# Optimization experiments

Hardware: AMD Instinct MI355X
Metric: run time of the kernel (lower is better)

Reference implementation:

```python
import jax, jax.numpy as jnp
import numpy as np
from jax import lax

B, NC, NF = 16, 1024, 4096   # clouds, coarse pts/cloud, fine pts/cloud
C_IN, C_SKIP, C_HID, K = 256, 128, 256, 3
BN_EPS = 1e-5


def setup_inputs() -> dict:
    key = jax.random.key(0)
    ks = jax.random.split(key, 12)
    inp = {
        "x": jax.random.normal(ks[0], (B * NC, C_IN), jnp.float32),
        "pos": jax.random.normal(ks[1], (B * NC, 3), jnp.float32),
        "batch": jnp.arange(B * NC, dtype=jnp.int64) // NC,
        "x_skip": jax.random.normal(ks[2], (B * NF, C_SKIP), jnp.float32),
        "pos_skip": jax.random.normal(ks[3], (B * NF, 3), jnp.float32),
        "batch_skip": jnp.arange(B * NF, dtype=jnp.int64) // NF,
    }
    d_in = C_IN + C_SKIP
    inp["W1"] = jax.random.normal(ks[4], (d_in, C_HID), jnp.float32) / np.sqrt(d_in)
    inp["b1"] = jnp.zeros((C_HID,), jnp.float32)
    inp["g1"] = jnp.ones((C_HID,), jnp.float32)
    inp["be1"] = jnp.zeros((C_HID,), jnp.float32)
    inp["W2"] = jax.random.normal(ks[5], (C_HID, C_HID), jnp.float32) / np.sqrt(C_HID)
    inp["b2"] = jnp.zeros((C_HID,), jnp.float32)
    inp["g2"] = jnp.ones((C_HID,), jnp.float32)
    inp["be2"] = jnp.zeros((C_HID,), jnp.float32)
    return inp


def _knn_interpolate(x, pos, pos_skip):
    # batches are contiguous equal-size -> reshape per cloud
    xb = x.reshape(B, NC, C_IN)
    pc = pos.reshape(B, NC, 3)
    pf = pos_skip.reshape(B, NF, 3)
    # squared distances [B, NF, NC]
    d2 = jnp.sum((pf[:, :, None, :] - pc[:, None, :, :]) ** 2, axis=-1)
    neg_d, idx = lax.top_k(-d2, K)                      # [B, NF, K]
    w = 1.0 / jnp.maximum(-neg_d, 1e-16)                # inverse-squared-distance weights
    feats = xb[jnp.arange(B)[:, None, None], idx]       # [B, NF, K, C_IN]
    out = jnp.sum(w[..., None] * feats, axis=2) / jnp.sum(w, axis=2, keepdims=True)
    return out.reshape(B * NF, C_IN)


def _mlp_layer(h, W, b, g, be):
    z = jax.nn.relu(h @ W + b)
    mean = jnp.mean(z, axis=0)
    var = jnp.mean((z - mean) ** 2, axis=0)            # biased var, as torch BN
    return (z - mean) * lax.rsqrt(var + BN_EPS) * g + be


def reference(x, pos, batch, x_skip, pos_skip, batch_skip,
              W1, b1, g1, be1, W2, b2, g2, be2):
    h = _knn_interpolate(x, pos, pos_skip)
    h = jnp.concatenate([h, x_skip], axis=1)            # [B*NF, C_IN+C_SKIP]
    h = _mlp_layer(h, W1, b1, g1, be1)
    h = _mlp_layer(h, W2, b2, g2, be2)
    return h
```

## Files before the change

kernel.cpp:

```cpp
#include <hip/hip_runtime.h>
#include <hip/hip_bf16.h>

#define NB    16
#define NC    1024
#define NF    4096
#define MROWS 65536
#define CIN   256
#define CSK   128
#define DIN   384
#define CHID  256
#define BN_EPS 1e-5f

typedef __attribute__((ext_vector_type(8))) short bf16x8;
typedef __attribute__((ext_vector_type(4))) float f32x4;
typedef __attribute__((ext_vector_type(2))) float f32x2;

__device__ __forceinline__ unsigned short f2bfu(float f) {
  __hip_bfloat16 h = __float2bfloat16(f);
  return __builtin_bit_cast(unsigned short, h);
}
__device__ __forceinline__ float bfu2f(unsigned short u) {
  unsigned int w = ((unsigned int)u) << 16;
  return __builtin_bit_cast(float, w);
}

__device__ __forceinline__ void load_lds16(const void* g, void* lds) {
  __builtin_amdgcn_global_load_lds(
      (const __attribute__((address_space(1))) unsigned int*)g,
      (__attribute__((address_space(3))) unsigned int*)lds, 16, 0, 0);
}

__device__ __forceinline__ void ins3(float d2, int j, float& b0, float& b1,
                                     float& b2v, int& i0, int& i1, int& i2) {
  const bool c0 = d2 < b0, c1 = d2 < b1, c2 = d2 < b2v;
  const float nb1 = __builtin_amdgcn_fmed3f(d2, b0, b1);
  const float nb2 = __builtin_amdgcn_fmed3f(d2, b1, b2v);
  i2  = c1 ? i1 : (c2 ? j : i2);
  i1  = c0 ? i0 : (c1 ? j : i1);
  i0  = c0 ? j : i0;
  b2v = nb2;
  b1  = nb1;
  b0  = fminf(d2, b0);
}

__global__ __launch_bounds__(512) void knn_interp_kernel(
    const float* __restrict__ x,
    const float* __restrict__ pos,
    const float* __restrict__ x_skip,
    const float* __restrict__ pos_skip,
    __hip_bfloat16* __restrict__ h0,
    const float* __restrict__ W1,
    __hip_bfloat16* __restrict__ W1t,
    float* __restrict__ stats)
{
  const int tid = threadIdx.x, wid = tid >> 6, lane = tid & 63;

  if (blockIdx.x >= 1024) {
    const int c = blockIdx.x - 1024;
    if (c == 0 && tid < 256) {
      for (int k = tid; k < 1024; k += 256) stats[k] = 0.f;
    }
    if (tid < 256)
      W1t[(size_t)tid * DIN + c] = __float2bfloat16(W1[(size_t)c * CHID + tid]);
    return;
  }

  __shared__ f32x4 nxy[512];
  __shared__ f32x2 nz[512];
  __shared__ float  md[8][64][3];
  __shared__ int    mi[8][64][3];
  __shared__ float  fw[64][3];
  __shared__ int    fi[64][3];

  const int f0 = blockIdx.x * 64;
  const int b  = f0 >> 12;

  const float* pb = pos + (size_t)b * NC * 3;
  for (int j = tid; j < 512; j += 512) {
    const float* p = pb + 6 * j;
    nxy[j] = (f32x4){-p[0], -p[3], -p[1], -p[4]};
    nz[j]  = (f32x2){-p[2], -p[5]};
  }
  __syncthreads();

  const int f = f0 + lane;
  const float* pf = pos_skip + (size_t)f * 3;
  const float fx = pf[0], fy = pf[1], fz = pf[2];
  const f32x4 fxxyy = (f32x4){fx, fx, fy, fy};
  const f32x2 fzz = (f32x2){fz, fz};

  float b0 = 3.4e38f, b1 = 3.4e38f, b2v = 3.4e38f;
  int   i0 = 0, i1 = 0, i2 = 0;
  const int pbase = wid * 64;
#pragma unroll 4
  for (int p = 0; p < 64; ++p) {
    const f32x4 cxy = nxy[pbase + p];
    const f32x2 cz  = nz[pbase + p];
    f32x2 d2;
    {
#pragma clang fp contract(off)
      const f32x4 dxy = fxxyy + cxy;
      const f32x4 sq  = dxy * dxy;
      const f32x2 sxy = (f32x2){sq[0], sq[1]} + (f32x2){sq[2], sq[3]};
      const f32x2 dz  = fzz + cz;
      d2 = sxy + dz * dz;
    }
    const int j = 2 * (pbase + p);
    ins3(d2[0], j,     b0, b1, b2v, i0, i1, i2);
    ins3(d2[1], j + 1, b0, b1, b2v, i0, i1, i2);
  }
  md[wid][lane][0] = b0;  md[wid][lane][1] = b1;  md[wid][lane][2] = b2v;
  mi[wid][lane][0] = i0;  mi[wid][lane][1] = i1;  mi[wid][lane][2] = i2;
  __syncthreads();

  if (wid == 0) {
#pragma unroll
    for (int q = 1; q < 8; ++q)
#pragma unroll
      for (int e = 0; e < 3; ++e)
        ins3(md[q][lane][e], mi[q][lane][e], b0, b1, b2v, i0, i1, i2);

    float w0 = 1.f / fmaxf(b0, 1e-16f);
    float w1 = 1.f / fmaxf(b1, 1e-16f);
    float w2 = 1.f / fmaxf(b2v, 1e-16f);
    const float inv = 1.f / (w0 + w1 + w2);
    fw[lane][0] = w0 * inv; fw[lane][1] = w1 * inv; fw[lane][2] = w2 * inv;
    fi[lane][0] = i0; fi[lane][1] = i1; fi[lane][2] = i2;
  }
  __syncthreads();

  for (int pp = 0; pp < 8; ++pp) {
    const int p = wid * 8 + pp;
    const float w0 = fw[p][0], w1 = fw[p][1], w2 = fw[p][2];
    const int j0 = fi[p][0], j1 = fi[p][1], j2 = fi[p][2];
    const float4* r0 = (const float4*)(x + (size_t)(b * NC + j0) * CIN);
    const float4* r1 = (const float4*)(x + (size_t)(b * NC + j1) * CIN);
    const float4* r2 = (const float4*)(x + (size_t)(b * NC + j2) * CIN);
    const float4 a0 = r0[lane], a1 = r1[lane], a2 = r2[lane];
    float4 v;
    v.x = w0 * a0.x + w1 * a1.x + w2 * a2.x;
    v.y = w0 * a0.y + w1 * a1.y + w2 * a2.y;
    v.z = w0 * a0.z + w1 * a1.z + w2 * a2.z;
    v.w = w0 * a0.w + w1 * a1.w + w2 * a2.w;
    __hip_bfloat16* orow = h0 + (size_t)(f0 + p) * DIN;
    ushort4 o;
    o.x = f2bfu(v.x); o.y = f2bfu(v.y); o.z = f2bfu(v.z); o.w = f2bfu(v.w);
    ((ushort4*)orow)[lane] = o;
    const float2 s = ((const float2*)(x_skip + (size_t)(f0 + p) * CSK))[lane];
    const unsigned int packed =
        ((unsigned int)f2bfu(s.y) << 16) | (unsigned int)f2bfu(s.x);
    ((unsigned int*)(orow + CIN))[lane] = packed;
  }
}

__global__ __launch_bounds__(256) void prep_w2b2_kernel(
    const float* __restrict__ W2, const float* __restrict__ stats,
    const float* __restrict__ g1, const float* __restrict__ be1,
    const float* __restrict__ b2, __hip_bfloat16* __restrict__ W2t,
    float* __restrict__ b2p) {
  const int n = blockIdx.x, c = threadIdx.x;
  const int wid = c >> 6, lane = c & 63;
  const float m = stats[c] * (1.f / MROWS);
  const float var = stats[256 + c] * (1.f / MROWS) - m * m;
  const float sc = g1[c] * rsqrtf(var + BN_EPS);
  const float sh = be1[c] - m * sc;
  const float w = W2[(size_t)c * CHID + n];
  W2t[(size_t)n * CHID + c] = __float2bfloat16(sc * w);
  float p = sh * w;
#pragma unroll
  for (int off = 32; off > 0; off >>= 1) p += __shfl_down(p, off);
  __shared__ float red4[4];
  if (lane == 0) red4[wid] = p;
  __syncthreads();
  if (c == 0) b2p[n] = red4[0] + red4[1] + red4[2] + red4[3] + b2[n];
}

template<int KD>
__global__ __launch_bounds__(512) void gemm_bias_relu(
    const __hip_bfloat16* __restrict__ A,
    const __hip_bfloat16* __restrict__ Bt,
    const float* __restrict__ bias,
    __hip_bfloat16* __restrict__ out,
    float* __restrict__ gsum,
    float* __restrict__ gsq)
{
  __shared__ __hip_bfloat16 As[2 * 128 * 32];
  __shared__ __hip_bfloat16 Bs[2 * 256 * 32];
  __shared__ float ssum[256], ssq[256];
  const int tid = threadIdx.x;
  const int wid = tid >> 6, lane = tid & 63;
  const int bm = blockIdx.x;
  const int wr = wid >> 2, wc = wid & 3;
  const int la = lane & 15, lk = lane >> 4;

  if (tid < 256) { ssum[tid] = 0.f; ssq[tid] = 0.f; }

  f32x4 acc[4][4] = {};

  const int rA = tid >> 2;
  const int c8 = (tid & 3) * 8;
  const __hip_bfloat16* gA  = A  + (size_t)(bm * 128 + rA) * KD + c8;
  const __hip_bfloat16* gB0 = Bt + (size_t)rA * KD + c8;
  const __hip_bfloat16* gB1 = Bt + (size_t)(128 + rA) * KD + c8;
  char* ldsA  = (char*)As + wid * 1024;
  char* ldsB0 = (char*)Bs + wid * 1024;

  load_lds16(gA,       ldsA);
  load_lds16(gB0,      ldsB0);
  load_lds16(gB1,      ldsB0 + 8192);
  __syncthreads();

  const int nIter = KD / 32;
  for (int it = 0; it < nIter; ++it) {
    const int cur = it & 1, nxt = cur ^ 1;
    if (it + 1 < nIter) {
      const int k1 = (it + 1) * 32;
      load_lds16(gA  + k1, ldsA  + nxt * 8192);
      load_lds16(gB0 + k1, ldsB0 + nxt * 16384);
      load_lds16(gB1 + k1, ldsB0 + nxt * 16384 + 8192);
    }
    const __hip_bfloat16* Acur = As + cur * 4096;
    const __hip_bfloat16* Bcur = Bs + cur * 8192;
    bf16x8 af[4], bfr[4];
#pragma unroll
    for (int m = 0; m < 4; ++m)
      af[m] = *(const bf16x8*)(Acur + (wr * 64 + m * 16 + la) * 32 + lk * 8);
#pragma unroll
    for (int n = 0; n < 4; ++n)
      bfr[n] = *(const bf16x8*)(Bcur + (wc * 64 + n * 16 + la) * 32 + lk * 8);
#pragma unroll
    for (int m = 0; m < 4; ++m)
#pragma unroll
      for (int n = 0; n < 4; ++n)
        acc[m][n] = __builtin_amdgcn_mfma_f32_16x16x32_bf16(
            af[m], bfr[n], acc[m][n], 0, 0, 0);
    __syncthreads();
  }

  const int rowBase = bm * 128 + wr * 64 + lk * 4;
#pragma unroll
  for (int n = 0; n < 4; ++n) {
    const int col = wc * 64 + n * 16 + la;
    const float bs = bias[col];
    float ls = 0.f, ls2 = 0.f;
#pragma unroll
    for (int m = 0; m < 4; ++m) {
      const int row = rowBase + m * 16;
#pragma unroll
      for (int j = 0; j < 4; ++j) {
        float v = acc[m][n][j] + bs;
        v = fmaxf(v, 0.f);
        ls += v; ls2 += v * v;
        out[(size_t)(row + j) * 256 + col] = __float2bfloat16(v);
      }
    }
    atomicAdd(&ssum[col], ls);
    atomicAdd(&ssq[col], ls2);
  }
  __syncthreads();
  if (tid < 256) {
    atomicAdd(&gsum[tid], ssum[tid]);
    atomicAdd(&gsq[tid], ssq[tid]);
  }
}

__global__ __launch_bounds__(256) void bn_apply_kernel(
    const __hip_bfloat16* __restrict__ Z, const float* __restrict__ stats,
    const float* __restrict__ g2, const float* __restrict__ be2,
    float* __restrict__ out) {
  __shared__ float ssc[256], ssh[256];
  const int t = threadIdx.x;
  {
    const float m = stats[t] * (1.f / MROWS);
    const float var = stats[256 + t] * (1.f / MROWS) - m * m;
    const float sc = g2[t] * rsqrtf(var + BN_EPS);
    ssc[t] = sc;
    ssh[t] = be2[t] - m * sc;
  }
  __syncthreads();
  const size_t i8 = (size_t)blockIdx.x * 256 + t;
  const uint4 raw = ((const uint4*)Z)[i8];
  const int c0 = (int)((i8 * 8) & 255);
  const float4 scA = *(const float4*)(ssc + c0);
  const float4 scB = *(const float4*)(ssc + c0 + 4);
  const float4 shA = *(const float4*)(ssh + c0);
  const float4 shB = *(const float4*)(ssh + c0 + 4);
  float4 oa, ob;
  oa.x = bfu2f((unsigned short)(raw.x & 0xffff)) * scA.x + shA.x;
  oa.y = bfu2f((unsigned short)(raw.x >> 16))    * scA.y + shA.y;
  oa.z = bfu2f((unsigned short)(raw.y & 0xffff)) * scA.z + shA.z;
  oa.w = bfu2f((unsigned short)(raw.y >> 16))    * scA.w + shA.w;
  ob.x = bfu2f((unsigned short)(raw.z & 0xffff)) * scB.x + shB.x;
  ob.y = bfu2f((unsigned short)(raw.z >> 16))    * scB.y + shB.y;
  ob.z = bfu2f((unsigned short)(raw.w & 0xffff)) * scB.z + shB.z;
  ob.w = bfu2f((unsigned short)(raw.w >> 16))    * scB.w + shB.w;
  ((float4*)(out))[i8 * 2]     = oa;
  ((float4*)(out))[i8 * 2 + 1] = ob;
}

extern "C" void kernel_launch(void* const* d_in, const int* in_sizes, int n_in,
                              void* d_out, int out_size, void* d_ws,
                              size_t ws_size, hipStream_t stream) {
  (void)in_sizes; (void)n_in; (void)out_size; (void)ws_size;
  const float* x        = (const float*)d_in[0];
  const float* pos      = (const float*)d_in[1];
  const float* x_skip   = (const float*)d_in[3];
  const float* pos_skip = (const float*)d_in[4];
  const float* W1  = (const float*)d_in[6];
  const float* b1  = (const float*)d_in[7];
  const float* g1  = (const float*)d_in[8];
  const float* be1 = (const float*)d_in[9];
  const float* W2  = (const float*)d_in[10];
  const float* b2  = (const float*)d_in[11];
  const float* g2  = (const float*)d_in[12];
  const float* be2 = (const float*)d_in[13];
  float* out = (float*)d_out;

  char* ws = (char*)d_ws;
  __hip_bfloat16* h0  = (__hip_bfloat16*)(ws);
  __hip_bfloat16* z2  = (__hip_bfloat16*)(ws);
  __hip_bfloat16* W1t = (__hip_bfloat16*)(ws + 50331648);
  __hip_bfloat16* z1  = (__hip_bfloat16*)(ws + 50528256);
  __hip_bfloat16* W2t = (__hip_bfloat16*)(ws + 84082688);
  float* b2p    = (float*)(ws + 84213760);
  float* stats  = (float*)(ws + 84214784);

  knn_interp_kernel<<<1408, 512, 0, stream>>>(x, pos, x_skip, pos_skip, h0,
                                              W1, W1t, stats);
  gemm_bias_relu<DIN><<<512, 512, 0, stream>>>(h0, W1t, b1, z1,
                                               stats, stats + 256);
  prep_w2b2_kernel<<<256, 256, 0, stream>>>(W2, stats, g1, be1, b2, W2t, b2p);
  gemm_bias_relu<CHID><<<512, 512, 0, stream>>>(z1, W2t, b2p, z2,
                                                stats + 512, stats + 768);
  bn_apply_kernel<<<8192, 256, 0, stream>>>(z2, stats + 512, g2, be2, out);
}
```

Before: 136.9 us.

## Fuse second GEMM with BatchNorm via cooperative grid sync; restructure KNN search

The second GEMM and the final BatchNorm apply now run in one cooperative kernel. Each block computes two 128-row tiles, keeps the activations in registers, accumulates column statistics, waits on a grid-wide sync, then writes the normalized fp32 output directly. This removes the bf16 z2 round trip and one launch. The KNN kernel is also restructured: each point is split across 8 lanes, lanes merge their top-3 lists with index tie-breaking, and blocks are smaller. The costs are heavy register pressure from two accumulator sets, the cooperative launch requirement (with a fallback path), and reduced parallelism of only 256 blocks for the second GEMM.

```diff
diff --git a/kernel.cpp b/kernel.cpp
--- a/kernel.cpp
+++ b/kernel.cpp
@@ -1,5 +1,8 @@
 #include <hip/hip_runtime.h>
 #include <hip/hip_bf16.h>
+#include <hip/hip_cooperative_groups.h>
+
+namespace cg = cooperative_groups;
 
 #define NB    16
 #define NC    1024
@@ -13,7 +16,6 @@
 
 typedef __attribute__((ext_vector_type(8))) short bf16x8;
 typedef __attribute__((ext_vector_type(4))) float f32x4;
-typedef __attribute__((ext_vector_type(2))) float f32x2;
 
 __device__ __forceinline__ unsigned short f2bfu(float f) {
   __hip_bfloat16 h = __float2bfloat16(f);
@@ -43,7 +45,22 @@
   b0  = fminf(d2, b0);
 }
 
-__global__ __launch_bounds__(512) void knn_interp_kernel(
+__device__ __forceinline__ void ins3tb(float d, int j, float& b0, float& b1,
+                                       float& b2v, int& i0, int& i1, int& i2) {
+  const bool c0 = (d < b0) || (d == b0 && j < i0);
+  const bool c1 = (d < b1) || (d == b1 && j < i1);
+  const bool c2 = (d < b2v) || (d == b2v && j < i2);
+  const float nb1 = __builtin_amdgcn_fmed3f(d, b0, b1);
+  const float nb2 = __builtin_amdgcn_fmed3f(d, b1, b2v);
+  i2  = c1 ? i1 : (c2 ? j : i2);
+  i1  = c0 ? i0 : (c1 ? j : i1);
+  i0  = c0 ? j : i0;
+  b2v = nb2;
+  b1  = nb1;
+  b0  = fminf(d, b0);
+}
+
+__global__ __launch_bounds__(256) void knn_interp_kernel(
     const float* __restrict__ x,
     const float* __restrict__ pos,
     const float* __restrict__ x_skip,
@@ -55,77 +72,81 @@
 {
   const int tid = threadIdx.x, wid = tid >> 6, lane = tid & 63;
 
-  if (blockIdx.x >= 1024) {
-    const int c = blockIdx.x - 1024;
-    if (c == 0 && tid < 256) {
+  if (blockIdx.x >= 2048) {
+    const int c = blockIdx.x - 2048;
+    if (c == 0) {
       for (int k = tid; k < 1024; k += 256) stats[k] = 0.f;
     }
-    if (tid < 256)
-      W1t[(size_t)tid * DIN + c] = __float2bfloat16(W1[(size_t)c * CHID + tid]);
+    W1t[(size_t)tid * DIN + c] = __float2bfloat16(W1[(size_t)c * CHID + tid]);
     return;
   }
 
-  __shared__ f32x4 nxy[512];
-  __shared__ f32x2 nz[512];
-  __shared__ float  md[8][64][3];
-  __shared__ int    mi[8][64][3];
-  __shared__ float  fw[64][3];
-  __shared__ int    fi[64][3];
-
-  const int f0 = blockIdx.x * 64;
+  __shared__ float4 cposI[NC];
+  __shared__ float  fw[32][3];
+  __shared__ int    fi[32][3];
+
+  const int f0 = blockIdx.x * 32;
   const int b  = f0 >> 12;
 
   const float* pb = pos + (size_t)b * NC * 3;
-  for (int j = tid; j < 512; j += 512) {
-    const float* p = pb + 6 * j;
-    nxy[j] = (f32x4){-p[0], -p[3], -p[1], -p[4]};
-    nz[j]  = (f32x2){-p[2], -p[5]};
-  }
-  __syncthreads();
-
-  const int f = f0 + lane;
-  const float* pf = pos_skip + (size_t)f * 3;
-  const float fx = pf[0], fy = pf[1], fz = pf[2];
-  const f32x4 fxxyy = (f32x4){fx, fx, fy, fy};
-  const f32x2 fzz = (f32x2){fz, fz};
-
-  float b0 = 3.4e38f, b1 = 3.4e38f, b2v = 3.4e38f;
-  int   i0 = 0, i1 = 0, i2 = 0;
-  const int pbase = wid * 64;
+  for (int j = tid; j < NC; j += 256) {
+    cposI[((j & 127) << 3) | (j >> 7)] =
+        make_float4(pb[3 * j], pb[3 * j + 1], pb[3 * j + 2], 0.f);
+  }
+  __syncthreads();
+
+  const int ll = lane & 7;
+  const int pl = wid * 8 + (lane >> 3);
+  const int f  = f0 + pl;
+  const float fx = pos_skip[(size_t)f * 3];
+  const float fy = pos_skip[(size_t)f * 3 + 1];
+  const float fz = pos_skip[(size_t)f * 3 + 2];
+  const int jb = ll * 128;
+
+  float a0 = 3.4e38f, a1 = 3.4e38f, a2 = 3.4e38f;
+  float c0 = 3.4e38f, c1 = 3.4e38f, c2 = 3.4e38f;
+  int ia0 = 0, ia1 = 0, ia2 = 0, ic0 = 0, ic1 = 0, ic2 = 0;
 #pragma unroll 4
-  for (int p = 0; p < 64; ++p) {
-    const f32x4 cxy = nxy[pbase + p];
-    const f32x2 cz  = nz[pbase + p];
-    f32x2 d2;
-    {
-#pragma clang fp contract(off)
-      const f32x4 dxy = fxxyy + cxy;
-      const f32x4 sq  = dxy * dxy;
-      const f32x2 sxy = (f32x2){sq[0], sq[1]} + (f32x2){sq[2], sq[3]};
-      const f32x2 dz  = fzz + cz;
-      d2 = sxy + dz * dz;
-    }
-    const int j = 2 * (pbase + p);
-    ins3(d2[0], j,     b0, b1, b2v, i0, i1, i2);
-    ins3(d2[1], j + 1, b0, b1, b2v, i0, i1, i2);
-  }
-  md[wid][lane][0] = b0;  md[wid][lane][1] = b1;  md[wid][lane][2] = b2v;
-  mi[wid][lane][0] = i0;  mi[wid][lane][1] = i1;  mi[wid][lane][2] = i2;
-  __syncthreads();
-
-  if (wid == 0) {
-#pragma unroll
-    for (int q = 1; q < 8; ++q)
-#pragma unroll
-      for (int e = 0; e < 3; ++e)
-        ins3(md[q][lane][e], mi[q][lane][e], b0, b1, b2v, i0, i1, i2);
-
-    float w0 = 1.f / fmaxf(b0, 1e-16f);
-    float w1 = 1.f / fmaxf(b1, 1e-16f);
-    float w2 = 1.f / fmaxf(b2v, 1e-16f);
+  for (int t = 0; t < 64; ++t) {
+    const float4 pA = cposI[t * 8 + ll];
+    const float4 pB = cposI[(t + 64) * 8 + ll];
+    const float dxA = __fsub_rn(fx, pA.x), dyA = __fsub_rn(fy, pA.y),
+                dzA = __fsub_rn(fz, pA.z);
+    const float dxB = __fsub_rn(fx, pB.x), dyB = __fsub_rn(fy, pB.y),
+                dzB = __fsub_rn(fz, pB.z);
+    const float d2A = __fadd_rn(
+        __fadd_rn(__fmul_rn(dxA, dxA), __fmul_rn(dyA, dyA)),
+        __fmul_rn(dzA, dzA));
+    const float d2B = __fadd_rn(
+        __fadd_rn(__fmul_rn(dxB, dxB), __fmul_rn(dyB, dyB)),
+        __fmul_rn(dzB, dzB));
+    ins3(d2A, jb + t,      a0, a1, a2, ia0, ia1, ia2);
+    ins3(d2B, jb + 64 + t, c0, c1, c2, ic0, ic1, ic2);
+  }
+  ins3(c0, ic0, a0, a1, a2, ia0, ia1, ia2);
+  ins3(c1, ic1, a0, a1, a2, ia0, ia1, ia2);
+  ins3(c2, ic2, a0, a1, a2, ia0, ia1, ia2);
+
+#pragma unroll
+  for (int mm = 1; mm <= 4; mm <<= 1) {
+    const float o0 = __shfl_xor(a0, mm);
+    const float o1 = __shfl_xor(a1, mm);
+    const float o2 = __shfl_xor(a2, mm);
+    const int oj0 = __shfl_xor(ia0, mm);
+    const int oj1 = __shfl_xor(ia1, mm);
+    const int oj2 = __shfl_xor(ia2, mm);
+    ins3tb(o0, oj0, a0, a1, a2, ia0, ia1, ia2);
+    ins3tb(o1, oj1, a0, a1, a2, ia0, ia1, ia2);
+    ins3tb(o2, oj2, a0, a1, a2, ia0, ia1, ia2);
+  }
+
+  if (ll == 0) {
+    float w0 = 1.f / fmaxf(a0, 1e-16f);
+    float w1 = 1.f / fmaxf(a1, 1e-16f);
+    float w2 = 1.f / fmaxf(a2, 1e-16f);
     const float inv = 1.f / (w0 + w1 + w2);
-    fw[lane][0] = w0 * inv; fw[lane][1] = w1 * inv; fw[lane][2] = w2 * inv;
-    fi[lane][0] = i0; fi[lane][1] = i1; fi[lane][2] = i2;
+    fw[pl][0] = w0 * inv; fw[pl][1] = w1 * inv; fw[pl][2] = w2 * inv;
+    fi[pl][0] = ia0; fi[pl][1] = ia1; fi[pl][2] = ia2;
   }
   __syncthreads();
 
@@ -136,12 +157,12 @@
     const float4* r0 = (const float4*)(x + (size_t)(b * NC + j0) * CIN);
     const float4* r1 = (const float4*)(x + (size_t)(b * NC + j1) * CIN);
     const float4* r2 = (const float4*)(x + (size_t)(b * NC + j2) * CIN);
-    const float4 a0 = r0[lane], a1 = r1[lane], a2 = r2[lane];
+    const float4 a0v = r0[lane], a1v = r1[lane], a2v = r2[lane];
     float4 v;
-    v.x = w0 * a0.x + w1 * a1.x + w2 * a2.x;
-    v.y = w0 * a0.y + w1 * a1.y + w2 * a2.y;
-    v.z = w0 * a0.z + w1 * a1.z + w2 * a2.z;
-    v.w = w0 * a0.w + w1 * a1.w + w2 * a2.w;
+    v.x = w0 * a0v.x + w1 * a1v.x + w2 * a2v.x;
+    v.y = w0 * a0v.y + w1 * a1v.y + w2 * a2v.y;
+    v.z = w0 * a0v.z + w1 * a1v.z + w2 * a2v.z;
+    v.w = w0 * a0v.w + w1 * a1v.w + w2 * a2v.w;
     __hip_bfloat16* orow = h0 + (size_t)(f0 + p) * DIN;
     ushort4 o;
     o.x = f2bfu(v.x); o.y = f2bfu(v.y); o.z = f2bfu(v.z); o.w = f2bfu(v.w);
@@ -205,9 +226,9 @@
   char* ldsA  = (char*)As + wid * 1024;
   char* ldsB0 = (char*)Bs + wid * 1024;
 
-  load_lds16(gA,       ldsA);
-  load_lds16(gB0,      ldsB0);
-  load_lds16(gB1,      ldsB0 + 8192);
+  load_lds16(gA,  ldsA);
+  load_lds16(gB0, ldsB0);
+  load_lds16(gB1, ldsB0 + 8192);
   __syncthreads();
 
   const int nIter = KD / 32;
@@ -261,6 +282,119 @@
   if (tid < 256) {
     atomicAdd(&gsum[tid], ssum[tid]);
     atomicAdd(&gsq[tid], ssq[tid]);
+  }
+}
+
+__device__ __forceinline__ void gemm_tile_256(
+    const __hip_bfloat16* __restrict__ A, const __hip_bfloat16* __restrict__ Bt,
+    int bm, __hip_bfloat16* As, __hip_bfloat16* Bs,
+    int tid, int wid, int wr, int wc, int la, int lk, f32x4 (&acc)[4][4]) {
+  const int rA = tid >> 2;
+  const int c8 = (tid & 3) * 8;
+  const __hip_bfloat16* gA  = A  + (size_t)(bm * 128 + rA) * CHID + c8;
+  const __hip_bfloat16* gB0 = Bt + (size_t)rA * CHID + c8;
+  const __hip_bfloat16* gB1 = Bt + (size_t)(128 + rA) * CHID + c8;
+  char* ldsA  = (char*)As + wid * 1024;
+  char* ldsB0 = (char*)Bs + wid * 1024;
+
+  load_lds16(gA,  ldsA);
+  load_lds16(gB0, ldsB0);
+  load_lds16(gB1, ldsB0 + 8192);
+  __syncthreads();
+
+  for (int it = 0; it < CHID / 32; ++it) {
+    const int cur = it & 1, nxt = cur ^ 1;
+    if (it + 1 < CHID / 32) {
+      const int k1 = (it + 1) * 32;
+      load_lds16(gA  + k1, ldsA  + nxt * 8192);
+      load_lds16(gB0 + k1, ldsB0 + nxt * 16384);
+      load_lds16(gB1 + k1, ldsB0 + nxt * 16384 + 8192);
+    }
+    const __hip_bfloat16* Acur = As + cur * 4096;
+    const __hip_bfloat16* Bcur = Bs + cur * 8192;
+    bf16x8 af[4], bfr[4];
+#pragma unroll
+    for (int m = 0; m < 4; ++m)
+      af[m] = *(const bf16x8*)(Acur + (wr * 64 + m * 16 + la) * 32 + lk * 8);
+#pragma unroll
+    for (int n = 0; n < 4; ++n)
+      bfr[n] = *(const bf16x8*)(Bcur + (wc * 64 + n * 16 + la) * 32 + lk * 8);
+#pragma unroll
+    for (int m = 0; m < 4; ++m)
+#pragma unroll
+      for (int n = 0; n < 4; ++n)
+        acc[m][n] = __builtin_amdgcn_mfma_f32_16x16x32_bf16(
+            af[m], bfr[n], acc[m][n], 0, 0, 0);
+    __syncthreads();
+  }
+}
+
+__global__ __launch_bounds__(512, 2) void gemm2_bn_fused(
+    const __hip_bfloat16* __restrict__ A,
+    const __hip_bfloat16* __restrict__ Bt,
+    const float* __restrict__ bias,
+    float* __restrict__ gsum, float* __restrict__ gsq,
+    const float* __restrict__ g2, const float* __restrict__ be2,
+    float* __restrict__ out)
+{
+  __shared__ __hip_bfloat16 As[2 * 128 * 32];
+  __shared__ __hip_bfloat16 Bs[2 * 256 * 32];
+  __shared__ float ssum[256], ssq[256];
+  const int tid = threadIdx.x;
+  const int wid = tid >> 6, lane = tid & 63;
+  const int wr = wid >> 2, wc = wid & 3;
+  const int la = lane & 15, lk = lane >> 4;
+  const int bmA = blockIdx.x * 2, bmB = bmA + 1;
+
+  if (tid < 256) { ssum[tid] = 0.f; ssq[tid] = 0.f; }
+
+  f32x4 accA[4][4] = {};
+  f32x4 accB[4][4] = {};
+  gemm_tile_256(A, Bt, bmA, As, Bs, tid, wid, wr, wc, la, lk, accA);
+  gemm_tile_256(A, Bt, bmB, As, Bs, tid, wid, wr, wc, la, lk, accB);
+
+#pragma unroll
+  for (int n = 0; n < 4; ++n) {
+    const int col = wc * 64 + n * 16 + la;
+    const float bs = bias[col];
+    float ls = 0.f, ls2 = 0.f;
+#pragma unroll
+    for (int m = 0; m < 4; ++m)
+#pragma unroll
+      for (int j = 0; j < 4; ++j) {
+        float vA = fmaxf(accA[m][n][j] + bs, 0.f);
+        float vB = fmaxf(accB[m][n][j] + bs, 0.f);
+        accA[m][n][j] = vA; accB[m][n][j] = vB;
+        ls += vA + vB; ls2 += vA * vA + vB * vB;
+      }
+    atomicAdd(&ssum[col], ls);
+    atomicAdd(&ssq[col], ls2);
+  }
+  __syncthreads();
+  if (tid < 256) {
+    atomicAdd(&gsum[tid], ssum[tid]);
+    atomicAdd(&gsq[tid], ssq[tid]);
+  }
+
+  cg::this_grid().sync();
+
+#pragma unroll
+  for (int n = 0; n < 4; ++n) {
+    const int col = wc * 64 + n * 16 + la;
+    const float m_ = gsum[col] * (1.f / MROWS);
+    const float var = gsq[col] * (1.f / MROWS) - m_ * m_;
+    const float sc = g2[col] * rsqrtf(var + BN_EPS);
+    const float sh = be2[col] - m_ * sc;
+    const int rbA = bmA * 128 + wr * 64 + lk * 4;
+    const int rbB = bmB * 128 + wr * 64 + lk * 4;
+#pragma unroll
+    for (int m = 0; m < 4; ++m) {
+#pragma unroll
+      for (int j = 0; j < 4; ++j) {
+        out[(size_t)(rbA + m * 16 + j) * 256 + col] = accA[m][n][j] * sc + sh;
+        out[(size_t)(rbB + m * 16 + j) * 256 + col] = accB[m][n][j] * sc + sh;
+      }
+    }
   }
 }
 
@@ -325,12 +459,29 @@
   float* b2p    = (float*)(ws + 84213760);
   float* stats  = (float*)(ws + 84214784);
 
-  knn_interp_kernel<<<1408, 512, 0, stream>>>(x, pos, x_skip, pos_skip, h0,
+  knn_interp_kernel<<<2432, 256, 0, stream>>>(x, pos, x_skip, pos_skip, h0,
                                               W1, W1t, stats);
   gemm_bias_relu<DIN><<<512, 512, 0, stream>>>(h0, W1t, b1, z1,
                                                stats, stats + 256);
   prep_w2b2_kernel<<<256, 256, 0, stream>>>(W2, stats, g1, be1, b2, W2t, b2p);
-  gemm_bias_relu<CHID><<<512, 512, 0, stream>>>(z1, W2t, b2p, z2,
-                                                stats + 512, stats + 768);
-  bn_apply_kernel<<<8192, 256, 0, stream>>>(z2, stats + 512, g2, be2, out);
-}
+
+  {
+    const __hip_bfloat16* a2 = z1;
+    const __hip_bfloat16* bt2 = W2t;
+    const float* bias2 = b2p;
+    float* gsum2 = stats + 512;
+    float* gsq2  = stats + 768;
+    void* args[] = {(void*)&a2, (void*)&bt2, (void*)&bias2,
+                    (void*)&gsum2, (void*)&gsq2,
+                    (void*)&g2, (void*)&be2, (void*)&out};
+    hipError_t e = hipLaunchCooperativeKernel((const void*)gemm2_bn_fused,
+                                              dim3(256), dim3(512), args, 0,
+                                              stream);
+    if (e != hipSuccess) {
+      (void)hipGetLastError();
+      gemm_bias_relu<CHID><<<512, 512, 0, stream>>>(z1, W2t, b2p, z2,
+                                                    stats + 512, stats + 768);
+      bn_apply_kernel<<<8192, 256, 0, stream>>>(z2, stats + 512, g2, be2, out);
+    }
+  }
+}
```

Result: slower. 155.9 us (+13.9%).

## Split kNN search across 8 lanes per point with shuffle-based top-3 merge

Applied to the files above, without the earlier changes.

Reworks the kNN interpolation kernel so each fine point is handled by 8 lanes, each scanning 128 coarse points with two independent top-3 chains, then merging via xor shuffles with index tie-breaking instead of LDS reductions and extra barriers. The full coarse cloud is staged in swizzled LDS, and blocks shrink to 256 threads covering 32 points each. The gather and write of features use wider per-lane vector stores. This removes the LDS merge stage and block-level syncs at the cost of more shuffle work and repeated position loads per block.

```diff
diff --git a/kernel.cpp b/kernel.cpp
--- a/kernel.cpp
+++ b/kernel.cpp
@@ -13,7 +13,6 @@
 
 typedef __attribute__((ext_vector_type(8))) short bf16x8;
 typedef __attribute__((ext_vector_type(4))) float f32x4;
-typedef __attribute__((ext_vector_type(2))) float f32x2;
 
 __device__ __forceinline__ unsigned short f2bfu(float f) {
   __hip_bfloat16 h = __float2bfloat16(f);
@@ -22,6 +21,9 @@
 __device__ __forceinline__ float bfu2f(unsigned short u) {
   unsigned int w = ((unsigned int)u) << 16;
   return __builtin_bit_cast(float, w);
+}
+__device__ __forceinline__ unsigned int pack2(float lo, float hi) {
+  return ((unsigned int)f2bfu(hi) << 16) | (unsigned int)f2bfu(lo);
 }
 
 __device__ __forceinline__ void load_lds16(const void* g, void* lds) {
@@ -43,7 +45,22 @@
   b0  = fminf(d2, b0);
 }
 
-__global__ __launch_bounds__(512) void knn_interp_kernel(
+__device__ __forceinline__ void ins3tb(float d, int j, float& b0, float& b1,
+                                       float& b2v, int& i0, int& i1, int& i2) {
+  const bool c0 = (d < b0) || (d == b0 && j < i0);
+  const bool c1 = (d < b1) || (d == b1 && j < i1);
+  const bool c2 = (d < b2v) || (d == b2v && j < i2);
+  const float nb1 = __builtin_amdgcn_fmed3f(d, b0, b1);
+  const float nb2 = __builtin_amdgcn_fmed3f(d, b1, b2v);
+  i2  = c1 ? i1 : (c2 ? j : i2);
+  i1  = c0 ? i0 : (c1 ? j : i1);
+  i0  = c0 ? j : i0;
+  b2v = nb2;
+  b1  = nb1;
+  b0  = fminf(d, b0);
+}
+
+__global__ __launch_bounds__(256) void knn_interp_kernel(
     const float* __restrict__ x,
     const float* __restrict__ pos,
     const float* __restrict__ x_skip,
@@ -53,103 +70,110 @@
     __hip_bfloat16* __restrict__ W1t,
     float* __restrict__ stats)
 {
-  const int tid = threadIdx.x, wid = tid >> 6, lane = tid & 63;
-
-  if (blockIdx.x >= 1024) {
-    const int c = blockIdx.x - 1024;
-    if (c == 0 && tid < 256) {
+  const int tid = threadIdx.x, lane = tid & 63, wid = tid >> 6;
+
+  if (blockIdx.x >= 2048) {
+    const int c = blockIdx.x - 2048;
+    if (c == 0) {
       for (int k = tid; k < 1024; k += 256) stats[k] = 0.f;
     }
-    if (tid < 256)
-      W1t[(size_t)tid * DIN + c] = __float2bfloat16(W1[(size_t)c * CHID + tid]);
+    W1t[(size_t)tid * DIN + c] = __float2bfloat16(W1[(size_t)c * CHID + tid]);
     return;
   }
 
-  __shared__ f32x4 nxy[512];
-  __shared__ f32x2 nz[512];
-  __shared__ float  md[8][64][3];
-  __shared__ int    mi[8][64][3];
-  __shared__ float  fw[64][3];
-  __shared__ int    fi[64][3];
-
-  const int f0 = blockIdx.x * 64;
+  __shared__ float4 cposI[NC];
+
+  const int f0 = blockIdx.x * 32;
   const int b  = f0 >> 12;
 
   const float* pb = pos + (size_t)b * NC * 3;
-  for (int j = tid; j < 512; j += 512) {
-    const float* p = pb + 6 * j;
-    nxy[j] = (f32x4){-p[0], -p[3], -p[1], -p[4]};
-    nz[j]  = (f32x2){-p[2], -p[5]};
-  }
-  __syncthreads();
-
-  const int f = f0 + lane;
-  const float* pf = pos_skip + (size_t)f * 3;
-  const float fx = pf[0], fy = pf[1], fz = pf[2];
-  const f32x4 fxxyy = (f32x4){fx, fx, fy, fy};
-  const f32x2 fzz = (f32x2){fz, fz};
-
-  float b0 = 3.4e38f, b1 = 3.4e38f, b2v = 3.4e38f;
-  int   i0 = 0, i1 = 0, i2 = 0;
-  const int pbase = wid * 64;
-#pragma unroll 4
-  for (int p = 0; p < 64; ++p) {
-    const f32x4 cxy = nxy[pbase + p];
-    const f32x2 cz  = nz[pbase + p];
-    f32x2 d2;
-    {
-#pragma clang fp contract(off)
-      const f32x4 dxy = fxxyy + cxy;
-      const f32x4 sq  = dxy * dxy;
-      const f32x2 sxy = (f32x2){sq[0], sq[1]} + (f32x2){sq[2], sq[3]};
-      const f32x2 dz  = fzz + cz;
-      d2 = sxy + dz * dz;
-    }
-    const int j = 2 * (pbase + p);
-    ins3(d2[0], j,     b0, b1, b2v, i0, i1, i2);
-    ins3(d2[1], j + 1, b0, b1, b2v, i0, i1, i2);
-  }
-  md[wid][lane][0] = b0;  md[wid][lane][1] = b1;  md[wid][lane][2] = b2v;
-  mi[wid][lane][0] = i0;  mi[wid][lane][1] = i1;  mi[wid][lane][2] = i2;
-  __syncthreads();
-
-  if (wid == 0) {
-#pragma unroll
-    for (int q = 1; q < 8; ++q)
-#pragma unroll
-      for (int e = 0; e < 3; ++e)
-        ins3(md[q][lane][e], mi[q][lane][e], b0, b1, b2v, i0, i1, i2);
-
-    float w0 = 1.f / fmaxf(b0, 1e-16f);
-    float w1 = 1.f / fmaxf(b1, 1e-16f);
-    float w2 = 1.f / fmaxf(b2v, 1e-16f);
-    const float inv = 1.f / (w0 + w1 + w2);
-    fw[lane][0] = w0 * inv; fw[lane][1] = w1 * inv; fw[lane][2] = w2 * inv;
-    fi[lane][0] = i0; fi[lane][1] = i1; fi[lane][2] = i2;
-  }
-  __syncthreads();
-
-  for (int pp = 0; pp < 8; ++pp) {
-    const int p = wid * 8 + pp;
-    const float w0 = fw[p][0], w1 = fw[p][1], w2 = fw[p][2];
-    const int j0 = fi[p][0], j1 = fi[p][1], j2 = fi[p][2];
-    const float4* r0 = (const float4*)(x + (size_t)(b * NC + j0) * CIN);
-    const float4* r1 = (const float4*)(x + (size_t)(b * NC + j1) * CIN);
-    const float4* r2 = (const float4*)(x + (size_t)(b * NC + j2) * CIN);
-    const float4 a0 = r0[lane], a1 = r1[lane], a2 = r2[lane];
+  for (int j = tid; j < NC; j += 256) {
+    const int slot = ((j & 127) << 3) | ((j >> 7) ^ (j & 7));
+    cposI[slot] = make_float4(pb[3 * j], pb[3 * j + 1], pb[3 * j + 2], 0.f);
+  }
+  __syncthreads();
+
+  const int ll = lane & 7;
+  const int pl = wid * 8 + (lane >> 3);
+  const int f  = f0 + pl;
+  const float fx = pos_skip[(size_t)f * 3];
+  const float fy = pos_skip[(size_t)f * 3 + 1];
+  const float fz = pos_skip[(size_t)f * 3 + 2];
+  const int jb = ll * 128;
+
+  float a0 = 3.4e38f, a1 = 3.4e38f, a2 = 3.4e38f;
+  float c0 = 3.4e38f, c1 = 3.4e38f, c2 = 3.4e38f;
+  int ia0 = 0, ia1 = 0, ia2 = 0, ic0 = 0, ic1 = 0, ic2 = 0;
+#pragma unroll 8
+  for (int t = 0; t < 64; ++t) {
+    const int sw = ll ^ (t & 7);
+    const float4 pA = cposI[t * 8 + sw];
+    const float4 pB = cposI[(t + 64) * 8 + sw];
+    const float dxA = __fsub_rn(fx, pA.x), dyA = __fsub_rn(fy, pA.y),
+                dzA = __fsub_rn(fz, pA.z);
+    const float dxB = __fsub_rn(fx, pB.x), dyB = __fsub_rn(fy, pB.y),
+                dzB = __fsub_rn(fz, pB.z);
+    const float d2A = __fadd_rn(
+        __fadd_rn(__fmul_rn(dxA, dxA), __fmul_rn(dyA, dyA)),
+        __fmul_rn(dzA, dzA));
+    const float d2B = __fadd_rn(
+        __fadd_rn(__fmul_rn(dxB, dxB), __fmul_rn(dyB, dyB)),
+        __fmul_rn(dzB, dzB));
+    ins3(d2A, jb + t,      a0, a1, a2, ia0, ia1, ia2);
+    ins3(d2B, jb + 64 + t, c0, c1, c2, ic0, ic1, ic2);
+  }
+  ins3(c0, ic0, a0, a1, a2, ia0, ia1, ia2);
+  ins3(c1, ic1, a0, a1, a2, ia0, ia1, ia2);
+  ins3(c2, ic2, a0, a1, a2, ia0, ia1, ia2);
+
+#pragma unroll
+  for (int mm = 1; mm <= 4; mm <<= 1) {
+    const float o0 = __shfl_xor(a0, mm);
+    const float o1 = __shfl_xor(a1, mm);
+    const float o2 = __shfl_xor(a2, mm);
+    const int oj0 = __shfl_xor(ia0, mm);
+    const int oj1 = __shfl_xor(ia1, mm);
+    const int oj2 = __shfl_xor(ia2, mm);
+    ins3tb(o0, oj0, a0, a1, a2, ia0, ia1, ia2);
+    ins3tb(o1, oj1, a0, a1, a2, ia0, ia1, ia2);
+    ins3tb(o2, oj2, a0, a1, a2, ia0, ia1, ia2);
+  }
+
+  float w0 = 1.f / fmaxf(a0, 1e-16f);
+  float w1 = 1.f / fmaxf(a1, 1e-16f);
+  float w2 = 1.f / fmaxf(a2, 1e-16f);
+  const float inv = 1.f / (w0 + w1 + w2);
+  w0 *= inv; w1 *= inv; w2 *= inv;
+
+  const float4* r0 = (const float4*)(x + (size_t)(b * NC + ia0) * CIN);
+  const float4* r1 = (const float4*)(x + (size_t)(b * NC + ia1) * CIN);
+  const float4* r2 = (const float4*)(x + (size_t)(b * NC + ia2) * CIN);
+  __hip_bfloat16* orow = h0 + (size_t)f * DIN;
+  unsigned int* o2u = (unsigned int*)orow;
+#pragma unroll
+  for (int k = 0; k < 8; ++k) {
+    const int fi4 = k * 8 + ll;
+    const float4 A = r0[fi4], B = r1[fi4], C = r2[fi4];
     float4 v;
-    v.x = w0 * a0.x + w1 * a1.x + w2 * a2.x;
-    v.y = w0 * a0.y + w1 * a1.y + w2 * a2.y;
-    v.z = w0 * a0.z + w1 * a1.z + w2 * a2.z;
-    v.w = w0 * a0.w + w1 * a1.w + w2 * a2.w;
-    __hip_bfloat16* orow = h0 + (size_t)(f0 + p) * DIN;
-    ushort4 o;
-    o.x = f2bfu(v.x); o.y = f2bfu(v.y); o.z = f2bfu(v.z); o.w = f2bfu(v.w);
-    ((ushort4*)orow)[lane] = o;
-    const float2 s = ((const float2*)(x_skip + (size_t)(f0 + p) * CSK))[lane];
-    const unsigned int packed =
-        ((unsigned int)f2bfu(s.y) << 16) | (unsigned int)f2bfu(s.x);
-    ((unsigned int*)(orow + CIN))[lane] = packed;
+    v.x = w0 * A.x + w1 * B.x + w2 * C.x;
+    v.y = w0 * A.y + w1 * B.y + w2 * C.y;
+    v.z = w0 * A.z + w1 * B.z + w2 * C.z;
+    v.w = w0 * A.w + w1 * B.w + w2 * C.w;
+    uint2 o;
+    o.x = pack2(v.x, v.y);
+    o.y = pack2(v.z, v.w);
+    ((uint2*)o2u)[fi4] = o;
+  }
+  const float4* xs = (const float4*)(x_skip + (size_t)f * CSK);
+  unsigned int* o2s = (unsigned int*)(orow + CIN);
+#pragma unroll
+  for (int k = 0; k < 4; ++k) {
+    const int fi4 = k * 8 + ll;
+    const float4 s = xs[fi4];
+    uint2 o;
+    o.x = pack2(s.x, s.y);
+    o.y = pack2(s.z, s.w);
+    ((uint2*)o2s)[fi4] = o;
   }
 }
 
@@ -205,9 +229,9 @@
   char* ldsA  = (char*)As + wid * 1024;
   char* ldsB0 = (char*)Bs + wid * 1024;
 
-  load_lds16(gA,       ldsA);
-  load_lds16(gB0,      ldsB0);
-  load_lds16(gB1,      ldsB0 + 8192);
+  load_lds16(gA,  ldsA);
+  load_lds16(gB0, ldsB0);
+  load_lds16(gB1, ldsB0 + 8192);
   __syncthreads();
 
   const int nIter = KD / 32;
@@ -325,7 +349,7 @@
   float* b2p    = (float*)(ws + 84213760);
   float* stats  = (float*)(ws + 84214784);
 
-  knn_interp_kernel<<<1408, 512, 0, stream>>>(x, pos, x_skip, pos_skip, h0,
+  knn_interp_kernel<<<2432, 256, 0, stream>>>(x, pos, x_skip, pos_skip, h0,
                                               W1, W1t, stats);
   gemm_bias_relu<DIN><<<512, 512, 0, stream>>>(h0, W1t, b1, z1,
                                                stats, stats + 256);
```

New measurement: 133.3 us. -2.6%, faster.
